# Performance work log

Hardware: AMD Instinct MI355X
Metric: run time of the kernel (lower is better)

The kernel has to match this reference:

```python
import jax, jax.numpy as jnp
import numpy as np


def _lem(x):
    # LEM with mix_margin=1: the depthwise 3x3 'conv' mask has exactly one
    # nonzero per channel, so it's a per-channel circular 1-pixel shift.
    # Channel index mod 5 determines direction:
    #   c%5==0: mask at (m, 2m) -> out(i,j)=x(i, j+1)  -> roll -1 along W
    #   c%5==1: mask at (m, 0)  -> out(i,j)=x(i, j-1)  -> roll +1 along W
    #   c%5==2: mask at (2m, m) -> out(i,j)=x(i+1, j)  -> roll -1 along H
    #   c%5==3: mask at (0, m)  -> out(i,j)=x(i-1, j)  -> roll +1 along H
    #   c%5==4: identity
    B, C, H, W = x.shape
    xr = x.reshape(B, C // 5, 5, H, W)
    out = jnp.stack([
        jnp.roll(xr[:, :, 0], -1, axis=-1),
        jnp.roll(xr[:, :, 1], 1, axis=-1),
        jnp.roll(xr[:, :, 2], -1, axis=-2),
        jnp.roll(xr[:, :, 3], 1, axis=-2),
        xr[:, :, 4],
    ], axis=2)
    return out.reshape(B, C, H, W)


def setup_inputs() -> dict:
    key = jax.random.key(0)
    x = jax.random.normal(key, (8, 320, 128, 128), dtype=jnp.float32)
    return {"x": x}


def reference(x):
    # Ablock spatial paradigm:
    # f = SiLU(lem0(x)); fatt = lem1(sigmoid(f) - 0.5); out = (f + x) * fatt
    f = jax.nn.silu(_lem(x))
    fatt = _lem(jax.nn.sigmoid(f) - 0.5)
    return (f + x) * fatt
```

## Files before the change

### kernel.cpp

```cpp
#include <hip/hip_runtime.h>


#define PLANE_ELEMS 16384
#define ROW_W 128

__device__ __forceinline__ float fast_sig(float z) {
    return __builtin_amdgcn_rcpf(1.0f + __expf(-z));
}
__device__ __forceinline__ float fast_silu(float z) {
    return z * fast_sig(z);
}

__global__ __launch_bounds__(256) void ablock_kernel(const float* __restrict__ x,
                                                     float* __restrict__ out,
                                                     int nv4) {
    int g = blockIdx.x * blockDim.x + threadIdx.x;
    if (g >= nv4) return;

    int plane = g >> 12;
    int o     = g & 4095;
    int row   = o >> 5;
    int c4    = o & 31;
    int col   = c4 << 2;
    int t     = plane % 5;

    const float*  p  = x + (size_t)plane * PLANE_ELEMS;
    const float4* p4 = (const float4*)p;
    int rowbase = row << 7;

    float4 x0 = p4[o];
    float4 x1, x2;

    if (t == 0) {
        float e4 = p[rowbase + ((col + 4) & 127)];
        float e5 = p[rowbase + ((col + 5) & 127)];
        x1 = make_float4(x0.y, x0.z, x0.w, e4);
        x2 = make_float4(x0.z, x0.w, e4, e5);
    } else if (t == 1) {
        float em1 = p[rowbase + ((col - 1) & 127)];
        float em2 = p[rowbase + ((col - 2) & 127)];
        x1 = make_float4(em1, x0.x, x0.y, x0.z);
        x2 = make_float4(em2, em1, x0.x, x0.y);
    } else if (t == 2) {
        x1 = p4[(((row + 1) & 127) << 5) + c4];
        x2 = p4[(((row + 2) & 127) << 5) + c4];
    } else if (t == 3) {
        x1 = p4[(((row - 1) & 127) << 5) + c4];
        x2 = p4[(((row - 2) & 127) << 5) + c4];
    } else {
        x1 = x0;
        x2 = x0;
    }

    float4 r;
    r.x = (fast_silu(x1.x) + x0.x) * (fast_sig(fast_silu(x2.x)) - 0.5f);
    r.y = (fast_silu(x1.y) + x0.y) * (fast_sig(fast_silu(x2.y)) - 0.5f);
    r.z = (fast_silu(x1.z) + x0.z) * (fast_sig(fast_silu(x2.z)) - 0.5f);
    r.w = (fast_silu(x1.w) + x0.w) * (fast_sig(fast_silu(x2.w)) - 0.5f);

    ((float4*)out)[g] = r;
}

extern "C" void kernel_launch(void* const* d_in, const int* in_sizes, int n_in,
                              void* d_out, int out_size, void* d_ws, size_t ws_size,
                              hipStream_t stream) {
    const float* x   = (const float*)d_in[0];
    float*       out = (float*)d_out;
    int n   = in_sizes[0];
    int nv4 = n >> 2;
    int block = 256;
    int grid  = (nv4 + block - 1) / block;
    ablock_kernel<<<grid, block, 0, stream>>>(x, out, nv4);
}
```

Baseline: 269.1 us.

## Use wavefront shuffles for horizontal neighbors, XCD block swizzle, nontemporal stores

Horizontal-shift channels now fetch their neighbor elements from adjacent lanes in the same row with __shfl instead of issuing two scalar global loads. Block IDs are remapped so each of the 8 XCDs handles a contiguous range of blocks, which should improve L2 locality for the vertical-neighbor row reloads. Output is written with nontemporal stores so it does not pollute the cache. Each 64-lane wavefront covers two complete 128-wide rows, so the shuffle wrap stays within the correct row.

```diff
diff --git a/kernel.cpp b/kernel.cpp
--- a/kernel.cpp
+++ b/kernel.cpp
@@ -2,7 +2,8 @@
 
 
 #define PLANE_ELEMS 16384
-#define ROW_W 128
+
+typedef float f32x4 __attribute__((ext_vector_type(4)));
 
 __device__ __forceinline__ float fast_sig(float z) {
     return __builtin_amdgcn_rcpf(1.0f + __expf(-z));
@@ -14,33 +15,40 @@
 __global__ __launch_bounds__(256) void ablock_kernel(const float* __restrict__ x,
                                                      float* __restrict__ out,
                                                      int nv4) {
-    int g = blockIdx.x * blockDim.x + threadIdx.x;
+    int bid = blockIdx.x;
+    int nb  = gridDim.x;
+    if ((nb & 7) == 0) {
+        int cpx = nb >> 3;
+        bid = (bid & 7) * cpx + (bid >> 3);
+    }
+
+    int g = bid * 256 + threadIdx.x;
     if (g >= nv4) return;
 
+    int lane  = threadIdx.x & 63;
     int plane = g >> 12;
     int o     = g & 4095;
     int row   = o >> 5;
     int c4    = o & 31;
-    int col   = c4 << 2;
     int t     = plane % 5;
 
-    const float*  p  = x + (size_t)plane * PLANE_ELEMS;
-    const float4* p4 = (const float4*)p;
-    int rowbase = row << 7;
+    const float4* p4 = (const float4*)(x + (size_t)plane * PLANE_ELEMS);
 
     float4 x0 = p4[o];
     float4 x1, x2;
 
     if (t == 0) {
-        float e4 = p[rowbase + ((col + 4) & 127)];
-        float e5 = p[rowbase + ((col + 5) & 127)];
-        x1 = make_float4(x0.y, x0.z, x0.w, e4);
-        x2 = make_float4(x0.z, x0.w, e4, e5);
+        int src  = (lane & 32) | ((lane + 1) & 31);
+        float nx = __shfl(x0.x, src, 64);
+        float ny = __shfl(x0.y, src, 64);
+        x1 = make_float4(x0.y, x0.z, x0.w, nx);
+        x2 = make_float4(x0.z, x0.w, nx, ny);
     } else if (t == 1) {
-        float em1 = p[rowbase + ((col - 1) & 127)];
-        float em2 = p[rowbase + ((col - 2) & 127)];
-        x1 = make_float4(em1, x0.x, x0.y, x0.z);
-        x2 = make_float4(em2, em1, x0.x, x0.y);
+        int src  = (lane & 32) | ((lane - 1) & 31);
+        float pw = __shfl(x0.w, src, 64);
+        float pz = __shfl(x0.z, src, 64);
+        x1 = make_float4(pw, x0.x, x0.y, x0.z);
+        x2 = make_float4(pz, pw, x0.x, x0.y);
     } else if (t == 2) {
         x1 = p4[(((row + 1) & 127) << 5) + c4];
         x2 = p4[(((row + 2) & 127) << 5) + c4];
@@ -52,13 +60,13 @@
         x2 = x0;
     }
 
-    float4 r;
+    f32x4 r;
     r.x = (fast_silu(x1.x) + x0.x) * (fast_sig(fast_silu(x2.x)) - 0.5f);
     r.y = (fast_silu(x1.y) + x0.y) * (fast_sig(fast_silu(x2.y)) - 0.5f);
     r.z = (fast_silu(x1.z) + x0.z) * (fast_sig(fast_silu(x2.z)) - 0.5f);
     r.w = (fast_silu(x1.w) + x0.w) * (fast_sig(fast_silu(x2.w)) - 0.5f);
 
-    ((float4*)out)[g] = r;
+    __builtin_nontemporal_store(r, (f32x4*)out + g);
 }
 
 extern "C" void kernel_launch(void* const* d_in, const int* in_sizes, int n_in,
```

New measurement: 273.8 us. About the same (+1.7%).

## Compute activations once per element and share neighbours via shuffles and LDS

Applied to the files above, without the earlier changes.

Each thread now computes silu and the gated sigmoid only for its own float4, and obtains shifted neighbours through wave shuffles for column shifts and through an LDS tile with halo rows for row shifts. This removes the redundant transcendental work and the extra global loads for neighbouring rows or columns. Blocks grow to 512 threads so each covers 16 full rows, and the bounds check is dropped on the assumption that the size divides evenly. The cost is a __syncthreads and a divergent halo-load path on the row-shift planes.

```diff
diff --git a/kernel.cpp b/kernel.cpp
--- a/kernel.cpp
+++ b/kernel.cpp
@@ -2,61 +2,93 @@
 
 
 #define PLANE_ELEMS 16384
-#define ROW_W 128
 
-__device__ __forceinline__ float fast_sig(float z) {
+__device__ __forceinline__ float fsig(float z) {
     return __builtin_amdgcn_rcpf(1.0f + __expf(-z));
 }
-__device__ __forceinline__ float fast_silu(float z) {
-    return z * fast_sig(z);
-}
 
-__global__ __launch_bounds__(256) void ablock_kernel(const float* __restrict__ x,
+__global__ __launch_bounds__(512) void ablock_kernel(const float* __restrict__ x,
                                                      float* __restrict__ out,
                                                      int nv4) {
-    int g = blockIdx.x * blockDim.x + threadIdx.x;
-    if (g >= nv4) return;
+    __shared__ float4 s_lds[18][32];
+    __shared__ float4 g_lds[18][32];
 
-    int plane = g >> 12;
-    int o     = g & 4095;
-    int row   = o >> 5;
-    int c4    = o & 31;
-    int col   = c4 << 2;
-    int t     = plane % 5;
+    const int tid   = threadIdx.x;
+    const int g     = blockIdx.x * 512 + tid;
+    const int lane  = tid & 63;
+    const int plane = g >> 12;
+    const int o     = g & 4095;
+    const int li    = tid >> 5;
+    const int c4    = tid & 31;
+    const int row   = o >> 5;
+    const int t     = plane % 5;
 
-    const float*  p  = x + (size_t)plane * PLANE_ELEMS;
-    const float4* p4 = (const float4*)p;
-    int rowbase = row << 7;
+    const float4* p4 = (const float4*)(x + (size_t)plane * PLANE_ELEMS);
+    const float4  x0 = p4[o];
 
-    float4 x0 = p4[o];
-    float4 x1, x2;
+    float4 s, gg;
+    s.x = x0.x * fsig(x0.x);  s.y = x0.y * fsig(x0.y);
+    s.z = x0.z * fsig(x0.z);  s.w = x0.w * fsig(x0.w);
+    gg.x = fsig(s.x) - 0.5f;  gg.y = fsig(s.y) - 0.5f;
+    gg.z = fsig(s.z) - 0.5f;  gg.w = fsig(s.w) - 0.5f;
+
+    float4 r;
 
     if (t == 0) {
-        float e4 = p[rowbase + ((col + 4) & 127)];
-        float e5 = p[rowbase + ((col + 5) & 127)];
-        x1 = make_float4(x0.y, x0.z, x0.w, e4);
-        x2 = make_float4(x0.z, x0.w, e4, e5);
+        int src = (lane & 32) | ((lane + 1) & 31);
+        float snx = __shfl(s.x,  src, 64);
+        float gnx = __shfl(gg.x, src, 64);
+        float gny = __shfl(gg.y, src, 64);
+        r.x = (s.y + x0.x) * gg.z;
+        r.y = (s.z + x0.y) * gg.w;
+        r.z = (s.w + x0.z) * gnx;
+        r.w = (snx + x0.w) * gny;
     } else if (t == 1) {
-        float em1 = p[rowbase + ((col - 1) & 127)];
-        float em2 = p[rowbase + ((col - 2) & 127)];
-        x1 = make_float4(em1, x0.x, x0.y, x0.z);
-        x2 = make_float4(em2, em1, x0.x, x0.y);
-    } else if (t == 2) {
-        x1 = p4[(((row + 1) & 127) << 5) + c4];
-        x2 = p4[(((row + 2) & 127) << 5) + c4];
-    } else if (t == 3) {
-        x1 = p4[(((row - 1) & 127) << 5) + c4];
-        x2 = p4[(((row - 2) & 127) << 5) + c4];
+        int src = (lane & 32) | ((lane - 1) & 31);
+        float spw = __shfl(s.w,  src, 64);
+        float gpz = __shfl(gg.z, src, 64);
+        float gpw = __shfl(gg.w, src, 64);
+        r.x = (spw + x0.x) * gpz;
+        r.y = (s.x + x0.y) * gpw;
+        r.z = (s.y + x0.z) * gg.x;
+        r.w = (s.z + x0.w) * gg.y;
+    } else if (t == 4) {
+        r.x = (s.x + x0.x) * gg.x;
+        r.y = (s.y + x0.y) * gg.y;
+        r.z = (s.z + x0.z) * gg.z;
+        r.w = (s.w + x0.w) * gg.w;
     } else {
-        x1 = x0;
-        x2 = x0;
+        const int base = (t == 2) ? li : li + 2;
+        s_lds[base][c4] = s;
+        g_lds[base][c4] = gg;
+
+        if (tid < 64) {
+            int k    = tid >> 5;
+            int hc4  = tid & 31;
+            int row0 = row - li;
+            int hidx, hrow;
+            if (t == 2) { hidx = 16 + k; hrow = (row0 + 16 + k) & 127; }
+            else        { hidx = k;      hrow = (row0 - 2 + k) & 127; }
+            float4 xh = p4[(hrow << 5) + hc4];
+            float4 hs, hg;
+            hs.x = xh.x * fsig(xh.x);  hs.y = xh.y * fsig(xh.y);
+            hs.z = xh.z * fsig(xh.z);  hs.w = xh.w * fsig(xh.w);
+            hg.x = fsig(hs.x) - 0.5f;  hg.y = fsig(hs.y) - 0.5f;
+            hg.z = fsig(hs.z) - 0.5f;  hg.w = fsig(hs.w) - 0.5f;
+            s_lds[hidx][hc4] = hs;
+            g_lds[hidx][hc4] = hg;
+        }
+        __syncthreads();
+
+        float4 s1 = s_lds[li + 1][c4];
+        float4 g2;
+        if (t == 2) g2 = g_lds[li + 2][c4];
+        else        g2 = g_lds[li][c4];
+        r.x = (s1.x + x0.x) * g2.x;
+        r.y = (s1.y + x0.y) * g2.y;
+        r.z = (s1.z + x0.z) * g2.z;
+        r.w = (s1.w + x0.w) * g2.w;
     }
-
-    float4 r;
-    r.x = (fast_silu(x1.x) + x0.x) * (fast_sig(fast_silu(x2.x)) - 0.5f);
-    r.y = (fast_silu(x1.y) + x0.y) * (fast_sig(fast_silu(x2.y)) - 0.5f);
-    r.z = (fast_silu(x1.z) + x0.z) * (fast_sig(fast_silu(x2.z)) - 0.5f);
-    r.w = (fast_silu(x1.w) + x0.w) * (fast_sig(fast_silu(x2.w)) - 0.5f);
 
     ((float4*)out)[g] = r;
 }
@@ -68,7 +100,7 @@
     float*       out = (float*)d_out;
     int n   = in_sizes[0];
     int nv4 = n >> 2;
-    int block = 256;
-    int grid  = (nv4 + block - 1) / block;
+    int block = 512;
+    int grid  = nv4 / block;
     ablock_kernel<<<grid, block, 0, stream>>>(x, out, nv4);
 }
```

Result: no change. 269.7 us, median of 2 (+0.2%).
